# Kernel tuning notes

Hardware: AMD Instinct MI355X
Metric: run time of the kernel (lower is better)

## Reference

```python
import jax, jax.numpy as jnp
import numpy as np

N_NODES = 50000
N_EDGES = 500000
N_GRAPHS = 256
D_IN, D_H1, D_H2, D_H3, D_OUT = 768, 256, 128, 64, 2


def _glorot(key, shape):
    fan_in, fan_out = shape[1], shape[0]
    lim = float(np.sqrt(6.0 / (fan_in + fan_out)))
    return jax.random.uniform(key, shape, jnp.float32, -lim, lim)


def setup_inputs() -> dict:
    key = jax.random.key(0)
    ks = jax.random.split(key, 12)
    x = jax.random.normal(ks[0], (N_NODES, D_IN), jnp.float32)
    edge_index = jax.random.randint(ks[1], (2, N_EDGES), 0, N_NODES, jnp.int64)
    batch = jnp.sort(jax.random.randint(ks[2], (N_NODES,), 0, N_GRAPHS, jnp.int64))
    return {
        "x": x,
        "edge_index": edge_index,
        "batch": batch,
        # SAGEConv1: out = lin_l(mean_aggr) + lin_r(x); bias only on lin_l (PyG default)
        "W1_l": _glorot(ks[3], (D_H1, D_IN)),
        "b1_l": jnp.zeros((D_H1,), jnp.float32),
        "W1_r": _glorot(ks[4], (D_H1, D_IN)),
        # SAGEConv2
        "W2_l": _glorot(ks[5], (D_H2, D_H1)),
        "b2_l": jnp.zeros((D_H2,), jnp.float32),
        "W2_r": _glorot(ks[6], (D_H2, D_H1)),
        # MLP head
        "W3": _glorot(ks[7], (D_H3, D_H2)),
        "b3": jnp.zeros((D_H3,), jnp.float32),
        "W4": _glorot(ks[8], (D_OUT, D_H3)),
        "b4": jnp.zeros((D_OUT,), jnp.float32),
    }


def _sage_conv(x, src, dst, deg_inv, W_l, b_l, W_r):
    # mean aggregation of neighbor features: scatter-add then divide by in-degree
    aggr = jax.ops.segment_sum(x[src], dst, num_segments=N_NODES)  # [N, d]
    aggr = aggr * deg_inv[:, None]
    return aggr @ W_l.T + b_l + x @ W_r.T


def reference(x, edge_index, batch, W1_l, b1_l, W1_r, W2_l, b2_l, W2_r, W3, b3, W4, b4):
    src, dst = edge_index[0], edge_index[1]
    deg = jax.ops.segment_sum(jnp.ones((N_EDGES,), x.dtype), dst, num_segments=N_NODES)
    deg_inv = jnp.where(deg > 0, 1.0 / jnp.maximum(deg, 1.0), 0.0)

    h = jax.nn.relu(_sage_conv(x, src, dst, deg_inv, W1_l, b1_l, W1_r))
    h = jax.nn.relu(_sage_conv(h, src, dst, deg_inv, W2_l, b2_l, W2_r))

    # global_mean_pool over graph ids
    pooled = jax.ops.segment_sum(h, batch, num_segments=N_GRAPHS)  # [G, 128]
    cnt = jax.ops.segment_sum(jnp.ones((N_NODES,), h.dtype), batch, num_segments=N_GRAPHS)
    pooled = pooled / jnp.maximum(cnt, 1.0)[:, None]

    # dropout is identity in eval mode
    h = pooled @ W3.T + b3
    h = h @ W4.T + b4
    return jax.nn.softmax(h, axis=-1)
```

## Files before the change

kernel.cpp:

```cpp
#include <hip/hip_runtime.h>
#include <cstdint>
#include <cstddef>

#define N_NODES 50000
#define N_EDGES 500000
#define N_GRAPHS 256
#define D_IN 768
#define D_H1 256
#define D_H2 128

typedef __attribute__((ext_vector_type(8))) __bf16 bf16x8;
typedef __attribute__((ext_vector_type(4))) float f32x4;

__device__ __forceinline__ float bf2f(uint32_t u) {
    union { uint32_t i; float f; } v; v.i = u << 16; return v.f;
}
__device__ __forceinline__ uint32_t f2bf(float f) {
    union { float f; uint32_t i; } v; v.f = f;
    uint32_t u = v.i;
    return (u + 0x7FFFu + ((u >> 16) & 1u)) >> 16;
}

__device__ __forceinline__ void pack_chunk(const float* __restrict__ p,
                                           uint16_t* __restrict__ out, int c) {
    float4 u = *(const float4*)p, v = *(const float4*)(p + 4);
    uint4 o;
    o.x = f2bf(u.x) | (f2bf(u.y) << 16);
    o.y = f2bf(u.z) | (f2bf(u.w) << 16);
    o.z = f2bf(v.x) | (f2bf(v.y) << 16);
    o.w = f2bf(v.z) | (f2bf(v.w) << 16);
    *(uint4*)(out + (size_t)c * 8) = o;
}

#define PACKA_BLKS 18750
#define PACKW1_BLKS 192
#define PACKW2_BLKS 32
#define HIST256 1954
__global__ __launch_bounds__(256) void k_pack_hist(
    const float* __restrict__ x, uint16_t* __restrict__ xp,
    const float* __restrict__ W1l, const float* __restrict__ W1r, uint16_t* __restrict__ W1p,
    const float* __restrict__ W2l, const float* __restrict__ W2r, uint16_t* __restrict__ W2p,
    const int* __restrict__ e_dst, int* __restrict__ deg)
{
    int b = blockIdx.x;
    if (b < PACKA_BLKS) {
        int c = b * 256 + threadIdx.x;
        int l = c & 63, t = c >> 6;
        int kt = t % 24, mt = t / 24;
        int fr = l & 15, fq = l >> 4;
        pack_chunk(x + (size_t)(mt * 16 + fr) * 768 + kt * 32 + fq * 8, xp, c);
    } else if (b < PACKA_BLKS + PACKW1_BLKS) {
        int c = (b - PACKA_BLKS) * 256 + threadIdx.x;
        int l = c & 63, t = c >> 6;
        int kt = t % 24, mt = t / 24;
        int fr = l & 15, fq = l >> 4;
        int row = mt * 16 + fr;
        const float* src = (row < 256) ? (W1l + (size_t)row * 768)
                                       : (W1r + (size_t)(row - 256) * 768);
        pack_chunk(src + kt * 32 + fq * 8, W1p, c);
    } else if (b < PACKA_BLKS + PACKW1_BLKS + PACKW2_BLKS) {
        int c = (b - PACKA_BLKS - PACKW1_BLKS) * 256 + threadIdx.x;
        int l = c & 63, t = c >> 6;
        int kt = t % 8, mt = t / 8;
        int fr = l & 15, fq = l >> 4;
        int row = mt * 16 + fr;
        const float* src = (row < 128) ? (W2l + (size_t)row * 256)
                                       : (W2r + (size_t)(row - 128) * 256);
        pack_chunk(src + kt * 32 + fq * 8, W2p, c);
    } else {
        int e = (b - PACKA_BLKS - PACKW1_BLKS - PACKW2_BLKS) * 256 + threadIdx.x;
        if (e < N_EDGES) atomicAdd(&deg[e_dst[e]], 1);
    }
}

__global__ __launch_bounds__(256) void k_scan(
    const int* __restrict__ deg, int* __restrict__ row_start, int* __restrict__ cursor,
    float* __restrict__ deg_inv, int* __restrict__ bsum, int n, int nb)
{
    __shared__ int buf[256];
    __shared__ int bbuf[256];
    int t = threadIdx.x, b = blockIdx.x, i = b * 256 + t;
    int v = (i < n) ? deg[i] : 0;
    buf[t] = v; __syncthreads();
    for (int off = 1; off < 256; off <<= 1) {
        int u = (t >= off) ? buf[t - off] : 0;
        __syncthreads(); buf[t] += u; __syncthreads();
    }
    if (t == 255) atomicExch(&bsum[b], buf[255] + 1);
    int w = 0;
    if (t < nb) {
        do { w = atomicAdd(&bsum[t], 0); } while (w == 0);
        w -= 1;
    }
    bbuf[t] = w; __syncthreads();
    for (int off = 1; off < 256; off <<= 1) {
        int u = (t >= off) ? bbuf[t - off] : 0;
        __syncthreads(); bbuf[t] += u; __syncthreads();
    }
    int base = (b > 0) ? bbuf[b - 1] : 0;
    if (i < n) {
        int rs = base + buf[t] - v;
        row_start[i] = rs;
        cursor[i] = rs;
        deg_inv[i] = (v > 0) ? (1.0f / (float)v) : 0.0f;
    }
    if (b == 0 && t == 0) row_start[n] = N_EDGES;
}

#define G1_BLKS 784
#define FILL_BLKS 1954
__global__ __launch_bounds__(256, 2) void k_gemm1_fill(
    const uint16_t* __restrict__ Ap, const uint16_t* __restrict__ Bp,
    uint16_t* __restrict__ Cl, uint16_t* __restrict__ Cr,
    const int* __restrict__ e_src, const int* __restrict__ e_dst,
    int* __restrict__ cursor, int* __restrict__ csr_src)
{
    if (blockIdx.x >= G1_BLKS) {
        int e = (blockIdx.x - G1_BLKS) * 256 + threadIdx.x;
        if (e < N_EDGES) {
            int d = e_dst[e];
            int pos = atomicAdd(&cursor[d], 1);
            csr_src[pos] = e_src[e];
        }
        return;
    }
    const int i = blockIdx.x;
    const int pr = (i >> 4) * 8 + (i & 7);
    const int half = (i >> 3) & 1;
    if (pr >= 391) return;
    const int KT = 24;
    const int tid = threadIdx.x;
    const int wave = tid >> 6, lane = tid & 63;
    const int fr = lane & 15, fq = lane >> 4;
    const int bm = pr * 128;
    const int wm = (wave >> 1) * 64, wn = (wave & 1) * 128;
    const int mtiles = (N_NODES + 15) >> 4;

    const bf16x8* ap[4];
    const bf16x8* bp[8];
    #pragma unroll
    for (int mi = 0; mi < 4; ++mi) {
        int mt = ((bm + wm) >> 4) + mi;
        if (mt > mtiles - 1) mt = mtiles - 1;
        ap[mi] = (const bf16x8*)Ap + (size_t)mt * KT * 64 + lane;
    }
    #pragma unroll
    for (int ni = 0; ni < 8; ++ni) {
        int nt = ((half * 256 + wn) >> 4) + ni;
        bp[ni] = (const bf16x8*)Bp + (size_t)nt * KT * 64 + lane;
    }

    f32x4 acc[4][8] = {};
    bf16x8 a0[4], b0[8], a1[4], b1[8];

    auto lA = [&](int kt, bf16x8* d) {
        #pragma unroll
        for (int mi = 0; mi < 4; ++mi) d[mi] = ap[mi][kt * 64];
    };
    auto lB = [&](int kt, bf16x8* d) {
        #pragma unroll
        for (int ni = 0; ni < 8; ++ni) d[ni] = bp[ni][kt * 64];
    };
    auto step = [&](bf16x8* a, bf16x8* b) {
        #pragma unroll
        for (int mi = 0; mi < 4; ++mi)
            #pragma unroll
            for (int ni = 0; ni < 8; ++ni)
                acc[mi][ni] = __builtin_amdgcn_mfma_f32_16x16x32_bf16(
                    a[mi], b[ni], acc[mi][ni], 0, 0, 0);
    };

    lA(0, a0); lB(0, b0);
    for (int ks = 0; ks < KT; ks += 2) {
        lA(ks + 1, a1); lB(ks + 1, b1);
        step(a0, b0);
        if (ks + 2 < KT) { lA(ks + 2, a0); lB(ks + 2, b0); }
        step(a1, b1);
    }

    uint16_t* __restrict__ C = half ? Cr : Cl;
    #pragma unroll
    for (int mi = 0; mi < 4; ++mi) {
        #pragma unroll
        for (int r = 0; r < 4; ++r) {
            int row = bm + wm + mi * 16 + fq * 4 + r;
            if (row >= N_NODES) continue;
            #pragma unroll
            for (int ni = 0; ni < 8; ++ni) {
                int col = wn + ni * 16 + fr;
                C[(size_t)row * 256 + col] = (uint16_t)f2bf(acc[mi][ni][r]);
            }
        }
    }
}

__global__ __launch_bounds__(256, 2) void k_mgemm(
    const uint16_t* __restrict__ Ap, const uint16_t* __restrict__ Bp,
    uint16_t* __restrict__ C, int M, int N, int KT)
{
    const int tid = threadIdx.x;
    const int wave = tid >> 6, lane = tid & 63;
    const int fr = lane & 15, fq = lane >> 4;
    const int bn = blockIdx.x * 256, bm = blockIdx.y * 128;
    const int wm = (wave >> 1) * 64, wn = (wave & 1) * 128;
    const int mtiles = (M + 15) >> 4;

    const bf16x8* ap[4];
    const bf16x8* bp[8];
    #pragma unroll
    for (int mi = 0; mi < 4; ++mi) {
        int mt = ((bm + wm) >> 4) + mi;
        if (mt > mtiles - 1) mt = mtiles - 1;
        ap[mi] = (const bf16x8*)Ap + (size_t)mt * KT * 64 + lane;
    }
    #pragma unroll
    for (int ni = 0; ni < 8; ++ni) {
        int nt = ((bn + wn) >> 4) + ni;
        bp[ni] = (const bf16x8*)Bp + (size_t)nt * KT * 64 + lane;
    }

    f32x4 acc[4][8] = {};
    bf16x8 a0[4], b0[8], a1[4], b1[8];

    auto lA = [&](int kt, bf16x8* d) {
        #pragma unroll
        for (int mi = 0; mi < 4; ++mi) d[mi] = ap[mi][kt * 64];
    };
    auto lB = [&](int kt, bf16x8* d) {
        #pragma unroll
        for (int ni = 0; ni < 8; ++ni) d[ni] = bp[ni][kt * 64];
    };
    auto step = [&](bf16x8* a, bf16x8* b) {
        #pragma unroll
        for (int mi = 0; mi < 4; ++mi)
            #pragma unroll
            for (int ni = 0; ni < 8; ++ni)
                acc[mi][ni] = __builtin_amdgcn_mfma_f32_16x16x32_bf16(
                    a[mi], b[ni], acc[mi][ni], 0, 0, 0);
    };

    lA(0, a0); lB(0, b0);
    for (int ks = 0; ks < KT; ks += 2) {
        lA(ks + 1, a1); lB(ks + 1, b1);
        step(a0, b0);
        if (ks + 2 < KT) { lA(ks + 2, a0); lB(ks + 2, b0); }
        step(a1, b1);
    }

    #pragma unroll
    for (int mi = 0; mi < 4; ++mi) {
        #pragma unroll
        for (int r = 0; r < 4; ++r) {
            int row = bm + wm + mi * 16 + fq * 4 + r;
            if (row >= M) continue;
            #pragma unroll
            for (int ni = 0; ni < 8; ++ni) {
                int col = bn + wn + ni * 16 + fr;
                C[(size_t)row * N + col] = (uint16_t)f2bf(acc[mi][ni][r]);
            }
        }
    }
}

__global__ __launch_bounds__(256) void k_agg1(
    const uint16_t* __restrict__ yl, const uint16_t* __restrict__ yr,
    const int* __restrict__ row_start, const int* __restrict__ csr,
    const float* __restrict__ deg_inv, const float* __restrict__ bias,
    uint16_t* __restrict__ h1p)
{
    int node = blockIdx.x * 8 + (threadIdx.x >> 5);
    if (node >= N_NODES) return;
    int c = threadIdx.x & 31;
    int s = row_start[node], e = row_start[node + 1];
    float a[8] = {};
    int p = s;
    auto accum = [&](uint4 t0) {
        a[0] += bf2f(t0.x & 0xFFFF); a[1] += bf2f(t0.x >> 16);
        a[2] += bf2f(t0.y & 0xFFFF); a[3] += bf2f(t0.y >> 16);
        a[4] += bf2f(t0.z & 0xFFFF); a[5] += bf2f(t0.z >> 16);
        a[6] += bf2f(t0.w & 0xFFFF); a[7] += bf2f(t0.w >> 16);
    };
    for (; p + 3 < e; p += 4) {
        uint4 t0 = *(const uint4*)(yl + (size_t)csr[p]     * 256 + c * 8);
        uint4 t1 = *(const uint4*)(yl + (size_t)csr[p + 1] * 256 + c * 8);
        uint4 t2 = *(const uint4*)(yl + (size_t)csr[p + 2] * 256 + c * 8);
        uint4 t3 = *(const uint4*)(yl + (size_t)csr[p + 3] * 256 + c * 8);
        accum(t0); accum(t1); accum(t2); accum(t3);
    }
    for (; p < e; ++p)
        accum(*(const uint4*)(yl + (size_t)csr[p] * 256 + c * 8));
    float w = deg_inv[node];
    uint4 tx = *(const uint4*)(yr + (size_t)node * 256 + c * 8);
    float4 b0 = *(const float4*)(bias + c * 8);
    float4 b1 = *(const float4*)(bias + c * 8 + 4);
    float v0 = fmaxf(a[0] * w + bf2f(tx.x & 0xFFFF) + b0.x, 0.f);
    float v1 = fmaxf(a[1] * w + bf2f(tx.x >> 16)    + b0.y, 0.f);
    float v2 = fmaxf(a[2] * w + bf2f(tx.y & 0xFFFF) + b0.z, 0.f);
    float v3 = fmaxf(a[3] * w + bf2f(tx.y >> 16)    + b0.w, 0.f);
    float v4 = fmaxf(a[4] * w + bf2f(tx.z & 0xFFFF) + b1.x, 0.f);
    float v5 = fmaxf(a[5] * w + bf2f(tx.z >> 16)    + b1.y, 0.f);
    float v6 = fmaxf(a[6] * w + bf2f(tx.w & 0xFFFF) + b1.z, 0.f);
    float v7 = fmaxf(a[7] * w + bf2f(tx.w >> 16)    + b1.w, 0.f);
    uint4 o;
    o.x = f2bf(v0) | (f2bf(v1) << 16);
    o.y = f2bf(v2) | (f2bf(v3) << 16);
    o.z = f2bf(v4) | (f2bf(v5) << 16);
    o.w = f2bf(v6) | (f2bf(v7) << 16);
    uint32_t addr = (((node >> 4) * 8 + (c >> 2)) * 64 + (c & 3) * 16 + (node & 15));
    *(uint4*)(h1p + (size_t)addr * 8) = o;
}

__global__ __launch_bounds__(256) void k_agg2(
    const uint16_t* __restrict__ y, const int* __restrict__ row_start,
    const int* __restrict__ csr, const float* __restrict__ deg_inv,
    const float* __restrict__ bias, float* __restrict__ out)
{
    int node = blockIdx.x * 4 + (threadIdx.x >> 6);
    if (node >= N_NODES) return;
    int lane = threadIdx.x & 63;
    int s = row_start[node], e = row_start[node + 1];
    float a0 = 0.f, a1 = 0.f;
    int p = s;
    for (; p + 3 < e; p += 4) {
        uint32_t t0 = *(const uint32_t*)(y + (size_t)csr[p]     * 256 + lane * 2);
        uint32_t t1 = *(const uint32_t*)(y + (size_t)csr[p + 1] * 256 + lane * 2);
        uint32_t t2 = *(const uint32_t*)(y + (size_t)csr[p + 2] * 256 + lane * 2);
        uint32_t t3 = *(const uint32_t*)(y + (size_t)csr[p + 3] * 256 + lane * 2);
        a0 += bf2f(t0 & 0xFFFF) + bf2f(t1 & 0xFFFF) + bf2f(t2 & 0xFFFF) + bf2f(t3 & 0xFFFF);
        a1 += bf2f(t0 >> 16)    + bf2f(t1 >> 16)    + bf2f(t2 >> 16)    + bf2f(t3 >> 16);
    }
    for (; p < e; ++p) {
        uint32_t t0 = *(const uint32_t*)(y + (size_t)csr[p] * 256 + lane * 2);
        a0 += bf2f(t0 & 0xFFFF);
        a1 += bf2f(t0 >> 16);
    }
    float w = deg_inv[node];
    uint32_t tx = *(const uint32_t*)(y + (size_t)node * 256 + 128 + lane * 2);
    float2 b = *(const float2*)(bias + lane * 2);
    float2 o;
    o.x = fmaxf(a0 * w + bf2f(tx & 0xFFFF) + b.x, 0.f);
    o.y = fmaxf(a1 * w + bf2f(tx >> 16)    + b.y, 0.f);
    *(float2*)(out + (size_t)node * 128 + lane * 2) = o;
}

__global__ void k_poolhead(const float* __restrict__ h2, const int* __restrict__ batch,
                           const float* __restrict__ W3, const float* __restrict__ b3,
                           const float* __restrict__ W4, const float* __restrict__ b4,
                           float* __restrict__ out)
{
    int g = blockIdx.x;
    __shared__ int s_lo, s_hi;
    __shared__ float p[128];
    __shared__ float hid[64];
    __shared__ float logit[2];
    int t = threadIdx.x;
    if (t == 0) {
        int lo = 0, hi = N_NODES;
        while (lo < hi) { int m = (lo + hi) >> 1; if (batch[m] < g) lo = m + 1; else hi = m; }
        s_lo = lo;
        int lo2 = lo, hi2 = N_NODES;
        while (lo2 < hi2) { int m = (lo2 + hi2) >> 1; if (batch[m] < g + 1) lo2 = m + 1; else hi2 = m; }
        s_hi = lo2;
    }
    __syncthreads();
    float sum = 0.f;
    for (int i = s_lo; i < s_hi; ++i) sum += h2[(size_t)i * D_H2 + t];
    int cnt = s_hi - s_lo;
    p[t] = sum / (float)(cnt > 0 ? cnt : 1);
    __syncthreads();
    if (t < 64) {
        float s = b3[t];
        #pragma unroll 4
        for (int k = 0; k < 128; ++k) s = fmaf(p[k], W3[t * 128 + k], s);
        hid[t] = s;
    }
    __syncthreads();
    if (t < 2) {
        float l = b4[t];
        for (int k = 0; k < 64; ++k) l = fmaf(hid[k], W4[t * 64 + k], l);
        logit[t] = l;
    }
    __syncthreads();
    if (t == 0) {
        float m = fmaxf(logit[0], logit[1]);
        float e0 = expf(logit[0] - m), e1 = expf(logit[1] - m);
        float inv = 1.0f / (e0 + e1);
        out[g * 2 + 0] = e0 * inv;
        out[g * 2 + 1] = e1 * inv;
    }
}

extern "C" void kernel_launch(void* const* d_in, const int* in_sizes, int n_in,
                              void* d_out, int out_size, void* d_ws, size_t ws_size,
                              hipStream_t stream)
{
    const float* x     = (const float*)d_in[0];
    const int*   ei    = (const int*)d_in[1];
    const int*   batch = (const int*)d_in[2];
    const float* W1l   = (const float*)d_in[3];
    const float* b1l   = (const float*)d_in[4];
    const float* W1r   = (const float*)d_in[5];
    const float* W2l   = (const float*)d_in[6];
    const float* b2l   = (const float*)d_in[7];
    const float* W2r   = (const float*)d_in[8];
    const float* W3    = (const float*)d_in[9];
    const float* b3    = (const float*)d_in[10];
    const float* W4    = (const float*)d_in[11];
    const float* b4    = (const float*)d_in[12];
    float* out = (float*)d_out;

    const int* e_src = ei;
    const int* e_dst = ei + N_EDGES;

    char* ws = (char*)d_ws;
    size_t off = 0;
    auto alloc = [&](size_t bytes) -> void* {
        void* p = ws + off;
        off = (off + bytes + 255) & ~(size_t)255;
        return p;
    };
    int*      deg       = (int*)alloc((size_t)(N_NODES + 256) * 4);
    int*      bsum      = deg + N_NODES;
    int*      row_start = (int*)alloc((size_t)(N_NODES + 1) * 4);
    int*      cursor    = (int*)alloc((size_t)N_NODES * 4);
    int*      csr_src   = (int*)alloc((size_t)N_EDGES * 4);
    float*    deg_inv   = (float*)alloc((size_t)N_NODES * 4);
    uint16_t* W1p       = (uint16_t*)alloc((size_t)512 * 768 * 2);
    uint16_t* W2p       = (uint16_t*)alloc((size_t)256 * 256 * 2);
    uint16_t* xp        = (uint16_t*)alloc((size_t)N_NODES * D_IN * 2);
    uint16_t* y1        = (uint16_t*)alloc((size_t)N_NODES * 512 * 2);
    uint16_t* h1p       = (uint16_t*)alloc((size_t)N_NODES * 256 * 2);

    uint16_t* y1l = y1;
    uint16_t* y1r = y1 + (size_t)N_NODES * 256;
    uint16_t* y2 = xp;
    float*    h2 = (float*)(xp + (size_t)N_NODES * 256);

    hipMemsetAsync(deg, 0, (size_t)(N_NODES + 256) * 4, stream);

    k_pack_hist<<<PACKA_BLKS + PACKW1_BLKS + PACKW2_BLKS + HIST256, 256, 0, stream>>>(
        x, xp, W1l, W1r, W1p, W2l, W2r, W2p, e_dst, deg);

    int nscan = (N_NODES + 255) / 256;
    k_scan<<<nscan, 256, 0, stream>>>(deg, row_start, cursor, deg_inv, bsum, N_NODES, nscan);

    k_gemm1_fill<<<G1_BLKS + FILL_BLKS, 256, 0, stream>>>(
        xp, W1p, y1l, y1r, e_src, e_dst, cursor, csr_src);
    k_agg1<<<(N_NODES + 7) / 8, 256, 0, stream>>>(y1l, y1r, row_start, csr_src, deg_inv, b1l, h1p);

    dim3 g2(1, (N_NODES + 127) / 128);
    k_mgemm<<<g2, 256, 0, stream>>>(h1p, W2p, y2, N_NODES, 256, 8);
    k_agg2<<<(N_NODES + 3) / 4, 256, 0, stream>>>(y2, row_start, csr_src, deg_inv, b2l, h2);

    k_poolhead<<<N_GRAPHS, 128, 0, stream>>>(h2, batch, W3, b3, W4, b4, out);
}
```

Before: 481.9 us.

## Fuse degree scan into GEMM1/CSR-fill kernel and batch pack/hist work per thread

Folds the separate scan kernel into the GEMM1+fill launch: the first blocks do the prefix scan and signal a device-scope counter, and the fill blocks spin on it before scattering edges, while GEMM blocks run freely. This removes one kernel launch and lets the scan overlap GEMM work. The pack/hist kernel now processes four chunks or edges per thread, with histogram blocks placed first, to cut block count and expose more memory-level parallelism. It relies on the scan blocks being scheduled before the waiting fill blocks, which ordered dispatch normally ensures but is not guaranteed.

```diff
diff --git a/kernel.cpp b/kernel.cpp
--- a/kernel.cpp
+++ b/kernel.cpp
@@ -21,102 +21,138 @@
     return (u + 0x7FFFu + ((u >> 16) & 1u)) >> 16;
 }
 
-__device__ __forceinline__ void pack_chunk(const float* __restrict__ p,
-                                           uint16_t* __restrict__ out, int c) {
-    float4 u = *(const float4*)p, v = *(const float4*)(p + 4);
-    uint4 o;
-    o.x = f2bf(u.x) | (f2bf(u.y) << 16);
-    o.y = f2bf(u.z) | (f2bf(u.w) << 16);
-    o.z = f2bf(v.x) | (f2bf(v.y) << 16);
-    o.w = f2bf(v.z) | (f2bf(v.w) << 16);
-    *(uint4*)(out + (size_t)c * 8) = o;
-}
-
-#define PACKA_BLKS 18750
+#define HIST4_BLKS 489
+#define PACKA4_BLKS 4688
 #define PACKW1_BLKS 192
 #define PACKW2_BLKS 32
-#define HIST256 1954
+#define NCHUNK_A 4800000
 __global__ __launch_bounds__(256) void k_pack_hist(
     const float* __restrict__ x, uint16_t* __restrict__ xp,
     const float* __restrict__ W1l, const float* __restrict__ W1r, uint16_t* __restrict__ W1p,
     const float* __restrict__ W2l, const float* __restrict__ W2r, uint16_t* __restrict__ W2p,
     const int* __restrict__ e_dst, int* __restrict__ deg)
 {
-    int b = blockIdx.x;
-    if (b < PACKA_BLKS) {
-        int c = b * 256 + threadIdx.x;
-        int l = c & 63, t = c >> 6;
-        int kt = t % 24, mt = t / 24;
-        int fr = l & 15, fq = l >> 4;
-        pack_chunk(x + (size_t)(mt * 16 + fr) * 768 + kt * 32 + fq * 8, xp, c);
-    } else if (b < PACKA_BLKS + PACKW1_BLKS) {
-        int c = (b - PACKA_BLKS) * 256 + threadIdx.x;
-        int l = c & 63, t = c >> 6;
-        int kt = t % 24, mt = t / 24;
-        int fr = l & 15, fq = l >> 4;
-        int row = mt * 16 + fr;
+    int b = blockIdx.x, t = threadIdx.x;
+    if (b < HIST4_BLKS) {
+        int base = b * 1024 + t;
+        #pragma unroll
+        for (int j = 0; j < 4; ++j) {
+            int e = base + j * 256;
+            if (e < N_EDGES) atomicAdd(&deg[e_dst[e]], 1);
+        }
+    } else if (b < HIST4_BLKS + PACKA4_BLKS) {
+        int c0 = (b - HIST4_BLKS) * 1024 + t;
+        float4 u[4], v[4];
+        #pragma unroll
+        for (int j = 0; j < 4; ++j) {
+            int c = c0 + j * 256; if (c > NCHUNK_A - 1) c = NCHUNK_A - 1;
+            int l = c & 63, tt = c >> 6;
+            int kt = tt % 24, mt = tt / 24;
+            const float* p = x + (size_t)(mt * 16 + (l & 15)) * 768 + kt * 32 + (l >> 4) * 8;
+            u[j] = *(const float4*)p;
+            v[j] = *(const float4*)(p + 4);
+        }
+        #pragma unroll
+        for (int j = 0; j < 4; ++j) {
+            int c = c0 + j * 256; if (c > NCHUNK_A - 1) c = NCHUNK_A - 1;
+            uint4 o;
+            o.x = f2bf(u[j].x) | (f2bf(u[j].y) << 16);
+            o.y = f2bf(u[j].z) | (f2bf(u[j].w) << 16);
+            o.z = f2bf(v[j].x) | (f2bf(v[j].y) << 16);
+            o.w = f2bf(v[j].z) | (f2bf(v[j].w) << 16);
+            *(uint4*)(xp + (size_t)c * 8) = o;
+        }
+    } else if (b < HIST4_BLKS + PACKA4_BLKS + PACKW1_BLKS) {
+        int c = (b - HIST4_BLKS - PACKA4_BLKS) * 256 + t;
+        int l = c & 63, tt = c >> 6;
+        int kt = tt % 24, mt = tt / 24;
+        int row = mt * 16 + (l & 15);
         const float* src = (row < 256) ? (W1l + (size_t)row * 768)
                                        : (W1r + (size_t)(row - 256) * 768);
-        pack_chunk(src + kt * 32 + fq * 8, W1p, c);
-    } else if (b < PACKA_BLKS + PACKW1_BLKS + PACKW2_BLKS) {
-        int c = (b - PACKA_BLKS - PACKW1_BLKS) * 256 + threadIdx.x;
-        int l = c & 63, t = c >> 6;
-        int kt = t % 8, mt = t / 8;
-        int fr = l & 15, fq = l >> 4;
-        int row = mt * 16 + fr;
+        const float* p = src + kt * 32 + (l >> 4) * 8;
+        float4 u = *(const float4*)p, v = *(const float4*)(p + 4);
+        uint4 o;
+        o.x = f2bf(u.x) | (f2bf(u.y) << 16);
+        o.y = f2bf(u.z) | (f2bf(u.w) << 16);
+        o.z = f2bf(v.x) | (f2bf(v.y) << 16);
+        o.w = f2bf(v.z) | (f2bf(v.w) << 16);
+        *(uint4*)(W1p + (size_t)c * 8) = o;
+    } else {
+        int c = (b - HIST4_BLKS - PACKA4_BLKS - PACKW1_BLKS) * 256 + t;
+        int l = c & 63, tt = c >> 6;
+        int kt = tt % 8, mt = tt / 8;
+        int row = mt * 16 + (l & 15);
         const float* src = (row < 128) ? (W2l + (size_t)row * 256)
                                        : (W2r + (size_t)(row - 128) * 256);
-        pack_chunk(src + kt * 32 + fq * 8, W2p, c);
-    } else {
-        int e = (b - PACKA_BLKS - PACKW1_BLKS - PACKW2_BLKS) * 256 + threadIdx.x;
-        if (e < N_EDGES) atomicAdd(&deg[e_dst[e]], 1);
-    }
-}
-
-__global__ __launch_bounds__(256) void k_scan(
-    const int* __restrict__ deg, int* __restrict__ row_start, int* __restrict__ cursor,
-    float* __restrict__ deg_inv, int* __restrict__ bsum, int n, int nb)
-{
-    __shared__ int buf[256];
-    __shared__ int bbuf[256];
-    int t = threadIdx.x, b = blockIdx.x, i = b * 256 + t;
-    int v = (i < n) ? deg[i] : 0;
-    buf[t] = v; __syncthreads();
-    for (int off = 1; off < 256; off <<= 1) {
-        int u = (t >= off) ? buf[t - off] : 0;
-        __syncthreads(); buf[t] += u; __syncthreads();
-    }
-    if (t == 255) atomicExch(&bsum[b], buf[255] + 1);
-    int w = 0;
-    if (t < nb) {
-        do { w = atomicAdd(&bsum[t], 0); } while (w == 0);
-        w -= 1;
-    }
-    bbuf[t] = w; __syncthreads();
-    for (int off = 1; off < 256; off <<= 1) {
-        int u = (t >= off) ? bbuf[t - off] : 0;
-        __syncthreads(); bbuf[t] += u; __syncthreads();
-    }
-    int base = (b > 0) ? bbuf[b - 1] : 0;
-    if (i < n) {
-        int rs = base + buf[t] - v;
-        row_start[i] = rs;
-        cursor[i] = rs;
-        deg_inv[i] = (v > 0) ? (1.0f / (float)v) : 0.0f;
-    }
-    if (b == 0 && t == 0) row_start[n] = N_EDGES;
-}
-
+        const float* p = src + kt * 32 + (l >> 4) * 8;
+        float4 u = *(const float4*)p, v = *(const float4*)(p + 4);
+        uint4 o;
+        o.x = f2bf(u.x) | (f2bf(u.y) << 16);
+        o.y = f2bf(u.z) | (f2bf(u.w) << 16);
+        o.z = f2bf(v.x) | (f2bf(v.y) << 16);
+        o.w = f2bf(v.z) | (f2bf(v.w) << 16);
+        *(uint4*)(W2p + (size_t)c * 8) = o;
+    }
+}
+
+#define SCAN_BLKS 196
+#define G1_OFF  SCAN_BLKS
 #define G1_BLKS 784
+#define FILL_OFF (G1_OFF + G1_BLKS)
 #define FILL_BLKS 1954
-__global__ __launch_bounds__(256, 2) void k_gemm1_fill(
+__global__ __launch_bounds__(256, 2) void k_scan_gemm1_fill(
     const uint16_t* __restrict__ Ap, const uint16_t* __restrict__ Bp,
     uint16_t* __restrict__ Cl, uint16_t* __restrict__ Cr,
     const int* __restrict__ e_src, const int* __restrict__ e_dst,
-    int* __restrict__ cursor, int* __restrict__ csr_src)
-{
-    if (blockIdx.x >= G1_BLKS) {
-        int e = (blockIdx.x - G1_BLKS) * 256 + threadIdx.x;
+    const int* __restrict__ deg, int* __restrict__ row_start,
+    int* __restrict__ cursor, float* __restrict__ deg_inv,
+    int* __restrict__ bsum, int* __restrict__ scan_done,
+    int* __restrict__ csr_src)
+{
+    int t = threadIdx.x;
+    if (blockIdx.x < SCAN_BLKS) {
+        __shared__ int buf[256];
+        __shared__ int bbuf[256];
+        int b = blockIdx.x, i = b * 256 + t;
+        int v = (i < N_NODES) ? deg[i] : 0;
+        buf[t] = v; __syncthreads();
+        for (int off = 1; off < 256; off <<= 1) {
+            int u = (t >= off) ? buf[t - off] : 0;
+            __syncthreads(); buf[t] += u; __syncthreads();
+        }
+        if (t == 255) atomicExch(&bsum[b], buf[255] + 1);
+        int w = 0;
+        if (t < SCAN_BLKS) {
+            do { w = atomicAdd(&bsum[t], 0); } while (w == 0);
+            w -= 1;
+        }
+        bbuf[t] = w; __syncthreads();
+        for (int off = 1; off < 256; off <<= 1) {
+            int u = (t >= off) ? bbuf[t - off] : 0;
+            __syncthreads(); bbuf[t] += u; __syncthreads();
+        }
+        int base = (b > 0) ? bbuf[b - 1] : 0;
+        if (i < N_NODES) {
+            int rs = base + buf[t] - v;
+            row_start[i] = rs;
+            cursor[i] = rs;
+            deg_inv[i] = (v > 0) ? (1.0f / (float)v) : 0.0f;
+        }
+        if (b == 0 && t == 0) row_start[N_NODES] = N_EDGES;
+        __threadfence();
+        __syncthreads();
+        if (t == 0)
+            __hip_atomic_fetch_add(scan_done, 1, __ATOMIC_RELEASE, __HIP_MEMORY_SCOPE_AGENT);
+        return;
+    }
+    if (blockIdx.x >= FILL_OFF) {
+        if (t < 64) {
+            while (__hip_atomic_load(scan_done, __ATOMIC_ACQUIRE,
+                                     __HIP_MEMORY_SCOPE_AGENT) < SCAN_BLKS)
+                __builtin_amdgcn_s_sleep(8);
+        }
+        __syncthreads();
+        int e = (blockIdx.x - FILL_OFF) * 256 + t;
         if (e < N_EDGES) {
             int d = e_dst[e];
             int pos = atomicAdd(&cursor[d], 1);
@@ -124,13 +160,12 @@
         }
         return;
     }
-    const int i = blockIdx.x;
+    const int i = blockIdx.x - G1_OFF;
     const int pr = (i >> 4) * 8 + (i & 7);
     const int half = (i >> 3) & 1;
     if (pr >= 391) return;
     const int KT = 24;
-    const int tid = threadIdx.x;
-    const int wave = tid >> 6, lane = tid & 63;
+    const int wave = t >> 6, lane = t & 63;
     const int fr = lane & 15, fq = lane >> 4;
     const int bm = pr * 128;
     const int wm = (wave >> 1) * 64, wn = (wave & 1) * 128;
@@ -419,8 +454,9 @@
         off = (off + bytes + 255) & ~(size_t)255;
         return p;
     };
-    int*      deg       = (int*)alloc((size_t)(N_NODES + 256) * 4);
+    int*      deg       = (int*)alloc((size_t)(N_NODES + 256 + 64) * 4);
     int*      bsum      = deg + N_NODES;
+    int*      scan_done = bsum + 256;
     int*      row_start = (int*)alloc((size_t)(N_NODES + 1) * 4);
     int*      cursor    = (int*)alloc((size_t)N_NODES * 4);
     int*      csr_src   = (int*)alloc((size_t)N_EDGES * 4);
@@ -436,16 +472,14 @@
     uint16_t* y2 = xp;
     float*    h2 = (float*)(xp + (size_t)N_NODES * 256);
 
-    hipMemsetAsync(deg, 0, (size_t)(N_NODES + 256) * 4, stream);
-
-    k_pack_hist<<<PACKA_BLKS + PACKW1_BLKS + PACKW2_BLKS + HIST256, 256, 0, stream>>>(
+    hipMemsetAsync(deg, 0, (size_t)(N_NODES + 256 + 64) * 4, stream);
+
+    k_pack_hist<<<HIST4_BLKS + PACKA4_BLKS + PACKW1_BLKS + PACKW2_BLKS, 256, 0, stream>>>(
         x, xp, W1l, W1r, W1p, W2l, W2r, W2p, e_dst, deg);
 
-    int nscan = (N_NODES + 255) / 256;
-    k_scan<<<nscan, 256, 0, stream>>>(deg, row_start, cursor, deg_inv, bsum, N_NODES, nscan);
-
-    k_gemm1_fill<<<G1_BLKS + FILL_BLKS, 256, 0, stream>>>(
-        xp, W1p, y1l, y1r, e_src, e_dst, cursor, csr_src);
+    k_scan_gemm1_fill<<<FILL_OFF + FILL_BLKS, 256, 0, stream>>>(
+        xp, W1p, y1l, y1r, e_src, e_dst, deg, row_start, cursor, deg_inv,
+        bsum, scan_done, csr_src);
     k_agg1<<<(N_NODES + 7) / 8, 256, 0, stream>>>(y1l, y1r, row_start, csr_src, deg_inv, b1l, h1p);
 
     dim3 g2(1, (N_NODES + 127) / 128);
```

New measurement: 503.9 us. 4.6% more time.
